# Performance work log

Measured on AMD Instinct MI355X. Metric: run time of the kernel, lower is better.

Reference implementation:

```python
import jax, jax.numpy as jnp
import numpy as np

B, N, DIM = 2, 512, 512
HEADS, DIM_HEAD, MAX_LEN = 8, 64, 1024


def _skew(QEr):
    # pad last dim on the left by 1, reshape (n, n+1) -> (n+1, n), drop first row
    padded = jnp.pad(QEr, ((0, 0), (0, 0), (0, 0), (1, 0)))
    b, h, r, c = padded.shape
    return padded.reshape(b, h, c, r)[:, :, 1:, :]


def _fft_multiply_parallel(A, x):
    # A: [b,h,n,n] decay matrix; x: [b,h,n,d]
    b, h, n, d = x.shape
    # y = [last column of A, first row of A] -> [b,h,2n]
    y = jnp.concatenate([A[:, :, :, -1], A[:, :, 0, :]], axis=-1)
    v = jnp.concatenate([x, jnp.zeros_like(x)], axis=-2)  # zero-pad rows n -> 2n
    # Faithful to the original torch code: fftn over ALL axes (incl. batch/head),
    # then ifft over the LAST axis only, then slice back to n rows.
    H = jnp.fft.fftn(y)[:, :, :, None] * jnp.fft.fftn(v)
    return jnp.fft.ifft(H)[:, :, :n, :]


def _forward(x, Wq, Wk, Wv, Er):
    b, n, _ = x.shape

    def split_heads(t):
        return t.reshape(b, n, HEADS, DIM_HEAD).transpose(0, 2, 1, 3)  # [b,h,n,d]

    q = split_heads(x @ Wq)
    k = split_heads(x @ Wk)
    v = split_heads(x @ Wv)
    # global (Frobenius) norm over the full tensor, as torch.norm(t)
    q = q / jnp.linalg.norm(q)
    k = k / jnp.linalg.norm(k)
    q_ = jax.nn.elu(q)
    k_ = jax.nn.elu(k)

    Er_t = Er[MAX_LEN - n:, :].T        # [d, n]
    QEr = q @ Er_t                       # [b,h,n,n]
    c = jnp.exp(_skew(QEr))              # relative-position decay, [b,h,n,n]

    a_1 = jnp.einsum('bhnx,bhny->bhnxy', k_, v).reshape(b, HEADS, n, DIM_HEAD * DIM_HEAD)
    d_2 = _fft_multiply_parallel(c, k_)                                   # [b,h,n,d] complex
    d_1 = _fft_multiply_parallel(c, a_1).reshape(b, HEADS, n, DIM_HEAD, DIM_HEAD)

    top = jnp.einsum('bhnx,bhnyz->bhnz', q_, d_1)    # complex [b,h,n,d]
    bottom = jnp.einsum('bhnx,bhny->bhny', q_, d_2)  # complex [b,h,n,d]
    return top / bottom


def setup_inputs() -> dict:
    key = jax.random.key(0)
    k1, k2, k3, k4, k5 = jax.random.split(key, 5)
    s = jnp.float32(1.0 / np.sqrt(DIM))
    return {
        'x': jax.random.normal(k1, (B, N, DIM), dtype=jnp.float32),
        'Wq': jax.random.normal(k2, (DIM, HEADS * DIM_HEAD), dtype=jnp.float32) * s,
        'Wk': jax.random.normal(k3, (DIM, HEADS * DIM_HEAD), dtype=jnp.float32) * s,
        'Wv': jax.random.normal(k4, (DIM, HEADS * DIM_HEAD), dtype=jnp.float32) * s,
        'Er': jax.random.normal(k5, (MAX_LEN, DIM_HEAD), dtype=jnp.float32),
    }


def reference(x, Wq, Wk, Wv, Er):
    return _forward(x, Wq, Wk, Wv, Er)
```

## Files before the change

kernel.cpp:

```cpp
#include <hip/hip_runtime.h>
#include <math.h>


#define DIMX 512
#define NPOS 512
#define PADIDX(m) ((m) + ((m) >> 4))

__global__ __launch_bounds__(256)
void gemm_kv_kernel(const float* __restrict__ x,
                    const float* __restrict__ Wk,
                    const float* __restrict__ Wv,
                    float* __restrict__ K,
                    float* __restrict__ V,
                    float* __restrict__ partials)
{
    const int blk  = blockIdx.x;
    const int sel  = (blk >> 2) & 1;
    const int cg   = blk & 3;
    const int rt   = blk >> 3;
    const int row0 = rt * 16;
    const int col0 = cg * 128;
    const int t    = threadIdx.x;
    const int tc   = t & 31;
    const int tr   = t >> 5;
    const float* __restrict__ W   = sel ? Wv : Wk;
    float* __restrict__       Out = sel ? V  : K;

    __shared__ float xs[16][DIMX];
    __shared__ float red[4];

    #pragma unroll
    for (int j = 0; j < 8; ++j) {
        const int f = t + j * 256;
        const int row = f >> 7, c4 = f & 127;
        *(float4*)&xs[row][c4 * 4] = *(const float4*)&x[(size_t)(row0 + row) * DIMX + c4 * 4];
    }
    __syncthreads();

    const float* Wb = W + col0 + tc * 4;
    float4 wA[8], wB[8];
    #pragma unroll
    for (int j = 0; j < 8; ++j) wA[j] = *(const float4*)&Wb[(size_t)(j) * DIMX];
    #pragma unroll
    for (int j = 0; j < 8; ++j) wB[j] = *(const float4*)&Wb[(size_t)(8 + j) * DIMX];

    float acc[2][4] = {{0,0,0,0},{0,0,0,0}};
    const int r0 = tr * 2;

    #define COMPUTE_CHUNK(WREG, CH)                                            \
        {   float4 xv0a = *(const float4*)&xs[r0][(CH) * 8];                   \
            float4 xv0b = *(const float4*)&xs[r0][(CH) * 8 + 4];               \
            float4 xv1a = *(const float4*)&xs[r0 + 1][(CH) * 8];               \
            float4 xv1b = *(const float4*)&xs[r0 + 1][(CH) * 8 + 4];           \
            _Pragma("unroll")                                                  \
            for (int kk = 0; kk < 4; ++kk) {                                   \
                const float x0 = (&xv0a.x)[kk], x1 = (&xv1a.x)[kk];            \
                _Pragma("unroll")                                              \
                for (int cc = 0; cc < 4; ++cc) {                               \
                    acc[0][cc] = fmaf(x0, (&WREG[kk].x)[cc], acc[0][cc]);      \
                    acc[1][cc] = fmaf(x1, (&WREG[kk].x)[cc], acc[1][cc]);      \
                } }                                                            \
            _Pragma("unroll")                                                  \
            for (int kk = 0; kk < 4; ++kk) {                                   \
                const float x0 = (&xv0b.x)[kk], x1 = (&xv1b.x)[kk];            \
                _Pragma("unroll")                                              \
                for (int cc = 0; cc < 4; ++cc) {                               \
                    acc[0][cc] = fmaf(x0, (&WREG[kk + 4].x)[cc], acc[0][cc]);  \
                    acc[1][cc] = fmaf(x1, (&WREG[kk + 4].x)[cc], acc[1][cc]);  \
                } } }

    for (int ch = 0; ch < 64; ch += 2) {
        COMPUTE_CHUNK(wA, ch)
        if (ch < 62) {
            #pragma unroll
            for (int j = 0; j < 8; ++j)
                wA[j] = *(const float4*)&Wb[(size_t)((ch + 2) * 8 + j) * DIMX];
        }
        COMPUTE_CHUNK(wB, ch + 1)
        if (ch < 62) {
            #pragma unroll
            for (int j = 0; j < 8; ++j)
                wB[j] = *(const float4*)&Wb[(size_t)((ch + 3) * 8 + j) * DIMX];
        }
    }
    #undef COMPUTE_CHUNK

    float ss = 0.f;
    #pragma unroll
    for (int i = 0; i < 2; ++i) {
        const int row = row0 + r0 + i;
        const float4 o = make_float4(acc[i][0], acc[i][1], acc[i][2], acc[i][3]);
        *(float4*)&Out[(size_t)row * DIMX + col0 + tc * 4] = o;
        ss += o.x * o.x + o.y * o.y + o.z * o.z + o.w * o.w;
    }
    if (sel == 0) {
        #pragma unroll
        for (int off = 32; off > 0; off >>= 1)
            ss += __shfl_down(ss, off, 64);
        if ((t & 63) == 0) red[t >> 6] = ss;
        __syncthreads();
        if (t == 0) partials[blk] = red[0] + red[1] + red[2] + red[3];
    } else {
        if (t == 0) partials[blk] = 0.f;
    }
}

__device__ __constant__ float C8[8] = {
    1.f, 0.70710678118654752440f, 0.f, -0.70710678118654752440f,
   -1.f, -0.70710678118654752440f, 0.f, 0.70710678118654752440f };
__device__ __constant__ float S8[8] = {
    0.f, -0.70710678118654752440f, -1.f, -0.70710678118654752440f,
    0.f,  0.70710678118654752440f,  1.f,  0.70710678118654752440f };

__global__ __launch_bounds__(256)
void stage1_kernel(const float* __restrict__ K,
                   const float* __restrict__ V,
                   const float* __restrict__ partials,
                   float2* __restrict__ Gk,
                   float2* __restrict__ Gp)
{
    const int m = blockIdx.x;
    const int t = threadIdx.x;
    __shared__ float kk[2][8][64];
    __shared__ float pp[2][8][64];
    __shared__ float skp[16][4];
    __shared__ float sk[2][8];
    __shared__ float sred[4];

    float p = partials[t] + partials[t + 256];
    #pragma unroll
    for (int off = 32; off > 0; off >>= 1)
        p += __shfl_down(p, off, 64);
    if ((t & 63) == 0) sred[t >> 6] = p;
    __syncthreads();
    const float scale = (float)(1.0 / sqrt((double)sred[0] + (double)sred[1] +
                                           (double)sred[2] + (double)sred[3]));

    for (int e = t; e < 1024; e += 256) {
        const int b = e >> 9, rem = e & 511, h = rem >> 6, z = rem & 63;
        const size_t src = (size_t)(b * 512 + m) * DIMX + h * 64 + z;
        const float kv = K[src] * scale;
        kk[b][h][z] = kv > 0.f ? kv : expm1f(kv);
        pp[b][h][z] = V[src];
    }
    __syncthreads();
    if (t < 64) {
        const int bh = t >> 2, q = t & 3;
        float s = 0.f;
        #pragma unroll
        for (int zz = 0; zz < 16; ++zz) s += kk[bh >> 3][bh & 7][q * 16 + zz];
        skp[bh][q] = s;
    }
    __syncthreads();
    if (t < 16) sk[t >> 3][t & 7] = skp[t][0] + skp[t][1] + skp[t][2] + skp[t][3];
    __syncthreads();
    for (int e = t; e < 1024; e += 256) {
        const int b = e >> 9, rem = e & 511, h = rem >> 6, z = rem & 63;
        pp[b][h][z] *= sk[b][h];
    }
    __syncthreads();

    for (int e2 = t; e2 < 512; e2 += 256) {
        const int be = e2 >> 5;
        const int zp = e2 & 31;
        const int beta = be >> 3, eta = be & 7;
        float4 rk, rp;
        #pragma unroll
        for (int zz = 0; zz < 2; ++zz) {
            const int z = zp * 2 + zz;
            float gkr = 0.f, gki = 0.f, gpr = 0.f, gpi = 0.f;
            #pragma unroll
            for (int b = 0; b < 2; ++b) {
                const float sgn = (beta & b) ? -1.f : 1.f;
                #pragma unroll
                for (int h = 0; h < 8; ++h) {
                    const int ph = (eta * h) & 7;
                    const float cr = C8[ph], ci = S8[ph];
                    const float a = kk[b][h][z] * sgn;
                    gkr = fmaf(a, cr, gkr); gki = fmaf(a, ci, gki);
                    const float p2 = pp[b][h][z] * sgn;
                    gpr = fmaf(p2, cr, gpr); gpi = fmaf(p2, ci, gpi);
                }
            }
            if (zz == 0) { rk.x = gkr; rk.y = gki; rp.x = gpr; rp.y = gpi; }
            else         { rk.z = gkr; rk.w = gki; rp.z = gpr; rp.w = gpi; }
        }
        const size_t o = ((size_t)be * NPOS + m) * 64 + zp * 2;
        *(float4*)&Gk[o] = rk;
        *(float4*)&Gp[o] = rp;
    }
}

__global__ __launch_bounds__(256)
void fft_div_kernel(const float2* __restrict__ Gk,
                    const float2* __restrict__ Gp,
                    float* __restrict__ out, int out_cplx)
{
    const int blk = blockIdx.x;
    const int j  = blk & 7;
    const int l  = (blk >> 3) & 3;
    const int be = blk >> 5;
    const int zg = j * 4 + l;
    const int t  = threadIdx.x;

    __shared__ float2 g[4][1088];
    __shared__ float2 w[544];

    for (int jj = t; jj < 512; jj += 256) {
        double s, cc;
        sincos(-6.2831853071795864769 * (double)jj / 1024.0, &s, &cc);
        w[PADIDX(jj)] = make_float2((float)cc, (float)s);
    }
    __syncthreads();

    for (int e = t; e < 1024; e += 256) {
        const int a = e >> 9;
        const int m = e & 511;
        const float4 v4 = *(const float4*)&(a ? Gp : Gk)[((size_t)be * NPOS + m) * 64 + zg * 2];
        const float2 v0 = make_float2(v4.x, v4.y);
        const float2 v1 = make_float2(v4.z, v4.w);
        const float2 tw = w[PADIDX(m)];
        g[a * 2 + 0][PADIDX(m)] = v0;
        g[a * 2 + 1][PADIDX(m)] = v1;
        g[a * 2 + 0][PADIDX(m + 512)] = make_float2(v0.x * tw.x - v0.y * tw.y,
                                                    v0.x * tw.y + v0.y * tw.x);
        g[a * 2 + 1][PADIDX(m + 512)] = make_float2(v1.x * tw.x - v1.y * tw.y,
                                                    v1.x * tw.y + v1.y * tw.x);
    }
    __syncthreads();

    #pragma unroll
    for (int s = 1; s <= 9; ++s) {
        const int S = 512 >> s;
        const int lg = 9 - s;
        #pragma unroll
        for (int q = 0; q < 8; ++q) {
            const int B    = t + 256 * q;
            const int arr  = B >> 9;
            const int beta = B & 511;
            const int jb   = beta & (S - 1);
            const int seg  = beta >> lg;
            const int u    = (seg << (lg + 1)) + jb;
            const int v    = u + S;
            const float2 tw = w[PADIDX(jb << s)];
            const float2 A  = g[arr][PADIDX(u)];
            const float2 Bb = g[arr][PADIDX(v)];
            g[arr][PADIDX(u)] = make_float2(A.x + Bb.x, A.y + Bb.y);
            const float sr = A.x - Bb.x, si = A.y - Bb.y;
            g[arr][PADIDX(v)] = make_float2(sr * tw.x - si * tw.y,
                                            sr * tw.y + si * tw.x);
        }
        __syncthreads();
    }

    for (int e2 = t; e2 < 512; e2 += 256) {
        const int i  = e2;
        const int pi = PADIDX(2 * i);
        const int mu = (int)(__brev((unsigned)i) >> 23);
        float4 res;
        #pragma unroll
        for (int zi = 0; zi < 2; ++zi) {
            const float2 D  = g[zi][pi];
            const float2 Nm = g[2 + zi][pi];
            const float inv = 1.f / (D.x * D.x + D.y * D.y);
            const float rr = (Nm.x * D.x + Nm.y * D.y) * inv;
            const float ri = (Nm.y * D.x - Nm.x * D.y) * inv;
            if (zi == 0) { res.x = rr; res.y = ri; }
            else         { res.z = rr; res.w = ri; }
        }
        const size_t o = ((size_t)be * NPOS + mu) * 64 + zg * 2;
        if (out_cplx) {
            *(float4*)&((float2*)out)[o] = res;
        } else {
            out[o]     = res.x;
            out[o + 1] = res.z;
        }
    }
}

__global__ __launch_bounds__(256)
void mdft_fallback_kernel(const float2* __restrict__ Gk,
                          const float2* __restrict__ Gp,
                          float* __restrict__ out,
                          int out_cplx)
{
    const int blk = blockIdx.x;
    const int be = blk >> 6, z = blk & 63;
    const int t = threadIdx.x;
    __shared__ float2 gk[512];
    __shared__ float2 gp[512];
    __shared__ float2 w[1024];

    for (int m = t; m < 512; m += 256) {
        const size_t idx = ((size_t)be * NPOS + m) * 64 + z;
        gk[m] = Gk[idx];
        gp[m] = Gp[idx];
    }
    for (int jj = t; jj < 1024; jj += 256) {
        double s, c;
        sincos(-6.2831853071795864769 * (double)jj / 1024.0, &s, &c);
        w[jj] = make_float2((float)c, (float)s);
    }
    __syncthreads();

    #pragma unroll
    for (int half = 0; half < 2; ++half) {
        const int mu = t + half * 256;
        double dr = 0.0, di = 0.0, nr = 0.0, ni = 0.0;
        int idx = 0;
        for (int m = 0; m < 512; ++m) {
            const float2 tw = w[idx];
            idx = (idx + mu) & 1023;
            const float2 a = gk[m];
            dr += (double)(a.x * tw.x - a.y * tw.y);
            di += (double)(a.x * tw.y + a.y * tw.x);
            const float2 p = gp[m];
            nr += (double)(p.x * tw.x - p.y * tw.y);
            ni += (double)(p.x * tw.y + p.y * tw.x);
        }
        const double dmag = dr * dr + di * di;
        const double orr = (nr * dr + ni * di) / dmag;
        const double oii = (ni * dr - nr * di) / dmag;
        const size_t o = ((size_t)be * NPOS + mu) * 64 + z;
        if (out_cplx) {
            out[2 * o]     = (float)orr;
            out[2 * o + 1] = (float)oii;
        } else {
            out[o] = (float)orr;
        }
    }
}

extern "C" void kernel_launch(void* const* d_in, const int* in_sizes, int n_in,
                              void* d_out, int out_size, void* d_ws, size_t ws_size,
                              hipStream_t stream)
{
    const float* x  = (const float*)d_in[0];
    const float* Wk = (const float*)d_in[2];
    const float* Wv = (const float*)d_in[3];
    float* out = (float*)d_out;

    char* ws = (char*)d_ws;
    float*  K    = (float*)(ws);
    float*  V    = (float*)(ws + (size_t)2097152);
    float2* Gk   = (float2*)(ws + (size_t)4194304);
    float*  part = (float*)(ws + (size_t)8388608);
    const int out_cplx = (out_size >= 2 * 2 * 8 * 512 * 64) ? 1 : 0;

    const bool ws_big = (ws_size >= (size_t)8390656 + (size_t)4194304);
    float2* Gp = ws_big ? (float2*)(ws + (size_t)8390656)
                        : (float2*)d_out;

    hipLaunchKernelGGL(gemm_kv_kernel, dim3(512), dim3(256), 0, stream,
                       x, Wk, Wv, K, V, part);
    hipLaunchKernelGGL(stage1_kernel, dim3(512), dim3(256), 0, stream,
                       K, V, part, Gk, Gp);
    if (ws_big) {
        hipLaunchKernelGGL(fft_div_kernel, dim3(512), dim3(256), 0, stream,
                           Gk, Gp, out, out_cplx);
    } else {
        hipLaunchKernelGGL(mdft_fallback_kernel, dim3(1024), dim3(256), 0, stream,
                           Gk, Gp, out, out_cplx);
    }
}
```

Measured before the change: 120.3 us.

## Compute K/V projection with split-bf16 MFMA instead of FP32 GEMM

Replaces the FP32 SIMT GEMM that produces K and V with a bf16 MFMA GEMM, using a hi/lo split (three MFMAs per product) to keep near-FP32 accuracy. Two new conversion kernels pre-split x and a transposed Wk/Wv into bf16 hi/lo buffers in workspace. The aim is to cut GEMM time by using matrix cores, at the cost of two extra launches, extra memory traffic, and slightly reduced precision. The new path runs only when the workspace is at least 20 MB; otherwise the old path is used.

```diff
diff --git a/kernel.cpp b/kernel.cpp
--- a/kernel.cpp
+++ b/kernel.cpp
@@ -5,6 +5,130 @@
 #define DIMX 512
 #define NPOS 512
 #define PADIDX(m) ((m) + ((m) >> 4))
+
+typedef unsigned short ushort_t;
+typedef unsigned int uint_t;
+typedef __bf16 bf16x8 __attribute__((ext_vector_type(8)));
+typedef float floatx4 __attribute__((ext_vector_type(4)));
+
+static __device__ inline ushort_t f2bf(float f) {
+    uint_t u = __float_as_uint(f);
+    u = u + 0x7FFFu + ((u >> 16) & 1u);
+    return (ushort_t)(u >> 16);
+}
+static __device__ inline float bf2f(ushort_t h) {
+    return __uint_as_float(((uint_t)h) << 16);
+}
+
+__global__ __launch_bounds__(256)
+void convx_kernel(const float* __restrict__ x,
+                  ushort_t* __restrict__ xh, ushort_t* __restrict__ xl)
+{
+    const int idx4 = blockIdx.x * 256 + threadIdx.x;
+    const float4 v = ((const float4*)x)[idx4];
+    ushort_t h[4], l[4];
+    const float vf[4] = {v.x, v.y, v.z, v.w};
+    #pragma unroll
+    for (int e = 0; e < 4; ++e) {
+        h[e] = f2bf(vf[e]);
+        l[e] = f2bf(vf[e] - bf2f(h[e]));
+    }
+    ushort_t* ph = xh + (size_t)idx4 * 4;
+    ushort_t* pl = xl + (size_t)idx4 * 4;
+    #pragma unroll
+    for (int e = 0; e < 4; ++e) { ph[e] = h[e]; pl[e] = l[e]; }
+}
+
+__global__ __launch_bounds__(256)
+void convw_kernel(const float* __restrict__ Wk, const float* __restrict__ Wv,
+                  ushort_t* __restrict__ wth, ushort_t* __restrict__ wtl)
+{
+    const int blk = blockIdx.x;
+    const int s  = blk >> 8;
+    const int kt = (blk >> 4) & 15;
+    const int nt = blk & 15;
+    const int t  = threadIdx.x;
+    const int c  = t & 31, r4 = t >> 5;
+    const float* __restrict__ W = s ? Wv : Wk;
+    __shared__ float tile[32][33];
+
+    #pragma unroll
+    for (int i = 0; i < 4; ++i) {
+        const int row = r4 + i * 8;
+        tile[row][c] = W[(size_t)(kt * 32 + row) * 512 + nt * 32 + c];
+    }
+    __syncthreads();
+    #pragma unroll
+    for (int i = 0; i < 4; ++i) {
+        const int nl = r4 + i * 8;
+        const float v = tile[c][nl];
+        const ushort_t h = f2bf(v);
+        const ushort_t l = f2bf(v - bf2f(h));
+        const size_t o = (size_t)(s * 512 + nt * 32 + nl) * 512 + kt * 32 + c;
+        wth[o] = h;
+        wtl[o] = l;
+    }
+}
+
+__global__ __launch_bounds__(256)
+void gemm_mfma_kernel(const ushort_t* __restrict__ xh, const ushort_t* __restrict__ xl,
+                      const ushort_t* __restrict__ wth, const ushort_t* __restrict__ wtl,
+                      float* __restrict__ K, float* __restrict__ V,
+                      float* __restrict__ partials)
+{
+    const int blk = blockIdx.x;
+    const int ct = blk >> 5;
+    const int rt = blk & 31;
+    const int t = threadIdx.x;
+    const int w = t >> 6, lane = t & 63;
+    const int qd = lane >> 4, lm = lane & 15;
+    const int mrow  = rt * 32 + (w >> 1) * 16 + lm;
+    const int ncol0 = ct * 64 + (w & 1) * 32;
+    const size_t aoff  = (size_t)mrow * 512 + qd * 8;
+    const size_t boff0 = (size_t)(ncol0 + lm) * 512 + qd * 8;
+    const size_t boff1 = (size_t)(ncol0 + 16 + lm) * 512 + qd * 8;
+
+    floatx4 acc0 = {0.f, 0.f, 0.f, 0.f};
+    floatx4 acc1 = {0.f, 0.f, 0.f, 0.f};
+
+    #pragma unroll
+    for (int ks = 0; ks < 16; ++ks) {
+        const int k0 = ks * 32;
+        const bf16x8 Ah  = *(const bf16x8*)&xh [aoff  + k0];
+        const bf16x8 Al  = *(const bf16x8*)&xl [aoff  + k0];
+        const bf16x8 B0h = *(const bf16x8*)&wth[boff0 + k0];
+        const bf16x8 B0l = *(const bf16x8*)&wtl[boff0 + k0];
+        const bf16x8 B1h = *(const bf16x8*)&wth[boff1 + k0];
+        const bf16x8 B1l = *(const bf16x8*)&wtl[boff1 + k0];
+        acc0 = __builtin_amdgcn_mfma_f32_16x16x32_bf16(Ah, B0h, acc0, 0, 0, 0);
+        acc0 = __builtin_amdgcn_mfma_f32_16x16x32_bf16(Ah, B0l, acc0, 0, 0, 0);
+        acc0 = __builtin_amdgcn_mfma_f32_16x16x32_bf16(Al, B0h, acc0, 0, 0, 0);
+        acc1 = __builtin_amdgcn_mfma_f32_16x16x32_bf16(Ah, B1h, acc1, 0, 0, 0);
+        acc1 = __builtin_amdgcn_mfma_f32_16x16x32_bf16(Ah, B1l, acc1, 0, 0, 0);
+        acc1 = __builtin_amdgcn_mfma_f32_16x16x32_bf16(Al, B1h, acc1, 0, 0, 0);
+    }
+
+    __shared__ float red[4];
+    float ss = 0.f;
+    const int orow0 = rt * 32 + (w >> 1) * 16 + qd * 4;
+    float* __restrict__ O = (ct < 8) ? K : V;
+    const int cb = (ct < 8) ? 0 : 512;
+    const int c0 = ncol0 + lm - cb;
+    #pragma unroll
+    for (int r = 0; r < 4; ++r) {
+        const size_t row = orow0 + r;
+        const float v0 = acc0[r], v1 = acc1[r];
+        O[row * 512 + c0]      = v0;
+        O[row * 512 + c0 + 16] = v1;
+        if (ct < 8) ss += v0 * v0 + v1 * v1;
+    }
+    #pragma unroll
+    for (int off = 32; off > 0; off >>= 1)
+        ss += __shfl_down(ss, off, 64);
+    if (lane == 0) red[w] = ss;
+    __syncthreads();
+    if (t == 0) partials[blk] = red[0] + red[1] + red[2] + red[3];
+}
 
 __global__ __launch_bounds__(256)
 void gemm_kv_kernel(const float* __restrict__ x,
@@ -347,18 +471,30 @@
     float*  part = (float*)(ws + (size_t)8388608);
     const int out_cplx = (out_size >= 2 * 2 * 8 * 512 * 64) ? 1 : 0;
 
-    const bool ws_big = (ws_size >= (size_t)8390656 + (size_t)4194304);
+    const bool ws_big = (ws_size >= (size_t)20971520);
     float2* Gp = ws_big ? (float2*)(ws + (size_t)8390656)
                         : (float2*)d_out;
 
-    hipLaunchKernelGGL(gemm_kv_kernel, dim3(512), dim3(256), 0, stream,
-                       x, Wk, Wv, K, V, part);
-    hipLaunchKernelGGL(stage1_kernel, dim3(512), dim3(256), 0, stream,
-                       K, V, part, Gk, Gp);
     if (ws_big) {
+        ushort_t* xh  = (ushort_t*)(ws + (size_t)16777216);
+        ushort_t* xl  = (ushort_t*)(ws + (size_t)17825792);
+        ushort_t* wth = (ushort_t*)(ws + (size_t)18874368);
+        ushort_t* wtl = (ushort_t*)(ws + (size_t)19922944);
+        hipLaunchKernelGGL(convx_kernel, dim3(512), dim3(256), 0, stream,
+                           x, xh, xl);
+        hipLaunchKernelGGL(convw_kernel, dim3(512), dim3(256), 0, stream,
+                           Wk, Wv, wth, wtl);
+        hipLaunchKernelGGL(gemm_mfma_kernel, dim3(512), dim3(256), 0, stream,
+                           xh, xl, wth, wtl, K, V, part);
+        hipLaunchKernelGGL(stage1_kernel, dim3(512), dim3(256), 0, stream,
+                           K, V, part, Gk, Gp);
         hipLaunchKernelGGL(fft_div_kernel, dim3(512), dim3(256), 0, stream,
                            Gk, Gp, out, out_cplx);
     } else {
+        hipLaunchKernelGGL(gemm_kv_kernel, dim3(512), dim3(256), 0, stream,
+                           x, Wk, Wv, K, V, part);
+        hipLaunchKernelGGL(stage1_kernel, dim3(512), dim3(256), 0, stream,
+                           K, V, part, Gk, Gp);
         hipLaunchKernelGGL(mdft_fallback_kernel, dim3(1024), dim3(256), 0, stream,
                            Gk, Gp, out, out_cplx);
     }
```

Measured after the change: 113.0 us. 1.06x faster.
